# Optimization experiments

Measured on AMD Instinct MI355X. Metric: run time of the kernel, lower is better.

The kernel has to match this reference:

```python
import jax, jax.numpy as jnp
import numpy as np

N_HEAD = 16
E = 1024
B, T = 2, 2048


def setup_inputs() -> dict:
    key = jax.random.key(0)
    ks = jax.random.split(key, 5)
    s = 1.0 / np.sqrt(E)
    return {
        "x": jax.random.normal(ks[0], (B, T, E), dtype=jnp.float32),
        "w_qkv": jax.random.normal(ks[1], (E, 3 * E), dtype=jnp.float32) * s,
        "b_qkv": jnp.zeros((3 * E,), dtype=jnp.float32),
        "w_proj": jax.random.normal(ks[2], (E, E), dtype=jnp.float32) * s,
        "b_proj": jnp.zeros((E,), dtype=jnp.float32),
    }


def reference(x, w_qkv, b_qkv, w_proj, b_proj):
    Bsz, Tlen, Emb = x.shape
    hd = Emb // N_HEAD
    qkv = x @ w_qkv + b_qkv  # [B, T, 3E]
    q, k, v = jnp.split(qkv, 3, axis=-1)
    # [B, H, T, hd]
    q = q.reshape(Bsz, Tlen, N_HEAD, hd).transpose(0, 2, 1, 3)
    k = k.reshape(Bsz, Tlen, N_HEAD, hd).transpose(0, 2, 1, 3)
    v = v.reshape(Bsz, Tlen, N_HEAD, hd).transpose(0, 2, 1, 3)
    scale = 1.0 / jnp.sqrt(jnp.asarray(hd, dtype=x.dtype))
    scores = jnp.einsum("bhqd,bhkd->bhqk", q, k) * scale  # [B, H, T, T]
    causal = jnp.tril(jnp.ones((Tlen, Tlen), dtype=bool))
    scores = jnp.where(causal, scores, jnp.asarray(-jnp.inf, dtype=scores.dtype))
    attn = jax.nn.softmax(scores, axis=-1)
    y = jnp.einsum("bhqk,bhkd->bhqd", attn, v)  # [B, H, T, hd]
    y = y.transpose(0, 2, 1, 3).reshape(Bsz, Tlen, Emb)
    return y @ w_proj + b_proj
```

## Files before the change

kernel.cpp:

```cpp
#include <hip/hip_runtime.h>
#include <hip/hip_bf16.h>

typedef __hip_bfloat16 bf16;
typedef __attribute__((ext_vector_type(8))) short sh8;
typedef __attribute__((ext_vector_type(4))) float f32x4;

#define BB 2
#define TT 2048
#define EE 1024
#define NH 16
#define HD 64
#define M_ROWS (BB * TT)
#define PPAD 72

__device__ __forceinline__ float b2f(bf16 v) { return __bfloat162float(v); }
__device__ __forceinline__ bf16 f2b(float v) { return __float2bfloat16(v); }
__device__ __forceinline__ unsigned short f2bu(float v) {
    union { bf16 b; unsigned short u; } x; x.b = f2b(v); return x.u;
}

__device__ __forceinline__ void gl2lds16(const bf16* g, bf16* l) {
    __builtin_amdgcn_global_load_lds(
        (__attribute__((address_space(1))) void*)g,
        (__attribute__((address_space(3))) void*)l, 16, 0, 0);
}

__global__ __launch_bounds__(256) void prep(
    const float* __restrict__ x, bf16* __restrict__ xb,
    const float* __restrict__ Wq, bf16* __restrict__ Wqt,
    const float* __restrict__ Wp, bf16* __restrict__ Wpt) {
    const int bid = blockIdx.x;
    if (bid < 4096) {
        const int i = bid * 256 + threadIdx.x;
        const float4 v = ((const float4*)x)[i];
        ushort4 u;
        u.x = f2bu(v.x); u.y = f2bu(v.y); u.z = f2bu(v.z); u.w = f2bu(v.w);
        ((ushort4*)xb)[i] = u;
        return;
    }
    __shared__ float Ld[64][65];
    const float* src; bf16* dst; int ncols, nc0, kr0;
    if (bid < 4096 + 768) {
        const int t = bid - 4096;
        src = Wq; dst = Wqt; ncols = 3072;
        nc0 = (t % 48) * 64; kr0 = (t / 48) * 64;
    } else {
        const int t = bid - 4096 - 768;
        src = Wp; dst = Wpt; ncols = 1024;
        nc0 = (t % 16) * 64; kr0 = (t / 16) * 64;
    }
#pragma unroll
    for (int i = 0; i < 16; ++i) {
        const int e = threadIdx.x + i * 256;
        Ld[e >> 6][e & 63] = src[(size_t)(kr0 + (e >> 6)) * ncols + nc0 + (e & 63)];
    }
    __syncthreads();
#pragma unroll
    for (int i = 0; i < 16; ++i) {
        const int e = threadIdx.x + i * 256;
        const int r2 = e & 63, c2 = e >> 6;
        dst[(size_t)(nc0 + c2) * EE + kr0 + r2] = f2b(Ld[r2][c2]);
    }
}

__device__ __forceinline__ void mfma_gemm_core(
    const bf16* __restrict__ A, const bf16* __restrict__ Bt,
    int m0, int n0, f32x4 acc[4][4], bf16* Al, bf16* Bl) {
    const int tid = threadIdx.x, w = tid >> 6, lane = tid & 63;
    const int li = lane & 15, quad = lane >> 4;
    const int wm = (w & 1) * 64, wn = (w >> 1) * 64;
    const int srow = w * 32 + (lane >> 3);
    const int scol = (lane & 7) * 8;

#pragma unroll
    for (int mt = 0; mt < 4; ++mt)
#pragma unroll
        for (int nt = 0; nt < 4; ++nt) acc[mt][nt] = (f32x4){0.f, 0.f, 0.f, 0.f};

    for (int k0 = 0; k0 < EE; k0 += 64) {
        __syncthreads();
#pragma unroll
        for (int j = 0; j < 4; ++j) {
            const int row = srow + j * 8;
            const int sk = scol ^ ((row & 7) * 8);
            gl2lds16(A  + (size_t)(m0 + row) * EE + k0 + sk, Al + row * 64 + scol);
            gl2lds16(Bt + (size_t)(n0 + row) * EE + k0 + sk, Bl + row * 64 + scol);
        }
        __syncthreads();
#pragma unroll
        for (int ks = 0; ks < 2; ++ks) {
            const int kof = (ks * 32 + quad * 8) ^ ((li & 7) * 8);
            sh8 af[4], bv[4];
#pragma unroll
            for (int mt = 0; mt < 4; ++mt)
                af[mt] = *(const sh8*)(Al + (wm + mt * 16 + li) * 64 + kof);
#pragma unroll
            for (int nt = 0; nt < 4; ++nt)
                bv[nt] = *(const sh8*)(Bl + (wn + nt * 16 + li) * 64 + kof);
#pragma unroll
            for (int mt = 0; mt < 4; ++mt)
#pragma unroll
                for (int nt = 0; nt < 4; ++nt)
                    acc[mt][nt] = __builtin_amdgcn_mfma_f32_16x16x32_bf16(
                        af[mt], bv[nt], acc[mt][nt], 0, 0, 0);
        }
    }
}

__global__ __launch_bounds__(256) void gemm_qkv_mfma(
    const bf16* __restrict__ A, const bf16* __restrict__ Bt,
    const float* __restrict__ bias,
    bf16* __restrict__ Qb, bf16* __restrict__ Kb, bf16* __restrict__ Vb) {
    __shared__ bf16 Al[128 * 64];
    __shared__ bf16 Bl[128 * 64];
    f32x4 acc[4][4];
    const int m0 = blockIdx.y * 128, n0 = blockIdx.x * 128;
    mfma_gemm_core(A, Bt, m0, n0, acc, Al, Bl);

    const int tid = threadIdx.x, w = tid >> 6, lane = tid & 63;
    const int li = lane & 15, quad = lane >> 4;
    const int wm = (w & 1) * 64, wn = (w >> 1) * 64;
    const int which = n0 >> 10;

#pragma unroll
    for (int nt = 0; nt < 4; ++nt) {
        const int n = n0 + wn + nt * 16 + li;
        const int hseg = n & 1023;
        const int h = hseg >> 6, d = hseg & 63;
        const float bv = bias[n];
        if (which == 2) {
#pragma unroll
            for (int mt = 0; mt < 4; ++mt) {
                const int mb = m0 + wm + mt * 16 + quad * 4;
                const int b = mb >> 11, t = mb & (TT - 1);
                ushort4 u;
                u.x = f2bu(acc[mt][nt][0] + bv);
                u.y = f2bu(acc[mt][nt][1] + bv);
                u.z = f2bu(acc[mt][nt][2] + bv);
                u.w = f2bu(acc[mt][nt][3] + bv);
                *(ushort4*)(Vb + ((size_t)((b * NH + h) * HD + d)) * TT + t) = u;
            }
        } else {
            bf16* dst = (which == 0) ? Qb : Kb;
            const float scl = (which == 0) ? 0.125f : 1.0f;
#pragma unroll
            for (int mt = 0; mt < 4; ++mt)
#pragma unroll
                for (int r = 0; r < 4; ++r) {
                    const int m = m0 + wm + mt * 16 + quad * 4 + r;
                    const int b = m >> 11, t = m & (TT - 1);
                    dst[((size_t)(b * NH + h) * TT + t) * HD + d] =
                        f2b((acc[mt][nt][r] + bv) * scl);
                }
        }
    }
}

__global__ __launch_bounds__(256) void gemm_proj_mfma(
    const bf16* __restrict__ A, const bf16* __restrict__ Bt,
    const float* __restrict__ bias, float* __restrict__ C) {
    __shared__ bf16 Al[128 * 64];
    __shared__ bf16 Bl[128 * 64];
    f32x4 acc[4][4];
    const int m0 = blockIdx.y * 128, n0 = blockIdx.x * 128;
    mfma_gemm_core(A, Bt, m0, n0, acc, Al, Bl);

    const int tid = threadIdx.x, w = tid >> 6, lane = tid & 63;
    const int li = lane & 15, quad = lane >> 4;
    const int wm = (w & 1) * 64, wn = (w >> 1) * 64;

#pragma unroll
    for (int nt = 0; nt < 4; ++nt) {
        const int n = n0 + wn + nt * 16 + li;
        const float bv = bias[n];
#pragma unroll
        for (int mt = 0; mt < 4; ++mt)
#pragma unroll
            for (int r = 0; r < 4; ++r) {
                const int m = m0 + wm + mt * 16 + quad * 4 + r;
                C[(size_t)m * EE + n] = acc[mt][nt][r] + bv;
            }
    }
}

__global__ __launch_bounds__(256) void attn_mfma(
    const bf16* __restrict__ Q, const bf16* __restrict__ K,
    const bf16* __restrict__ Vt, bf16* __restrict__ Y) {
    __shared__ bf16 Kl[2][64 * 64];
    __shared__ bf16 Vl[2][64 * 64];
    __shared__ bf16 Pl[4][16 * PPAD];

    const int tid  = threadIdx.x;
    const int w    = tid >> 6;
    const int lane = tid & 63;
    const int li   = lane & 15;
    const int quad = lane >> 4;
    const int swz  = (li & 7) * 8;
    const int idx  = blockIdx.x;
    const int qb   = 31 - (idx >> 5);
    const int bh   = idx & 31;
    const int q0   = qb << 6;
    const int qw0  = q0 + w * 16;

    const bf16* Qb = Q  + (size_t)bh * TT * HD;
    const bf16* Kb = K  + (size_t)bh * TT * HD;
    const bf16* Vb = Vt + (size_t)bh * HD * TT;

    sh8 qf0 = *(const sh8*)(Qb + (size_t)(qw0 + li) * HD + quad * 8);
    sh8 qf1 = *(const sh8*)(Qb + (size_t)(qw0 + li) * HD + 32 + quad * 8);

    f32x4 o[4];
#pragma unroll
    for (int nt = 0; nt < 4; ++nt) o[nt] = (f32x4){0.f, 0.f, 0.f, 0.f};
    float lacc = 0.f;

    const int l8 = lane >> 3, l7 = lane & 7;
    const int gcol = ((l7 ^ l8) * 8);

    const int ntiles = qb + 1;
#pragma unroll
    for (int c = 0; c < 2; ++c) {
        const int rb = w * 16 + c * 8;
        gl2lds16(Kb + (size_t)(rb + l8) * HD + gcol, &Kl[0][rb * 64]);
        gl2lds16(Vb + (size_t)(rb + l8) * TT + gcol, &Vl[0][rb * 64]);
    }

    for (int it = 0; it < ntiles; ++it) {
        const int cur = it & 1;
        __syncthreads();
        if (it + 1 < ntiles) {
            const int j1 = (it + 1) << 6;
            const int nxt = cur ^ 1;
#pragma unroll
            for (int c = 0; c < 2; ++c) {
                const int rb = w * 16 + c * 8;
                gl2lds16(Kb + (size_t)(j1 + rb + l8) * HD + gcol, &Kl[nxt][rb * 64]);
                gl2lds16(Vb + (size_t)(rb + l8) * TT + j1 + gcol, &Vl[nxt][rb * 64]);
            }
        }
        const bf16* kb = &Kl[cur][0];
        const bf16* vb = &Vl[cur][0];

        const bool diag = (it == ntiles - 1);
#pragma unroll
        for (int nt = 0; nt < 4; ++nt) {
            f32x4 a = (f32x4){0.f, 0.f, 0.f, 0.f};
            sh8 kf0 = *(const sh8*)(kb + (nt * 16 + li) * 64 + ((quad * 8) ^ swz));
            a = __builtin_amdgcn_mfma_f32_16x16x32_bf16(kf0, qf0, a, 0, 0, 0);
            sh8 kf1 = *(const sh8*)(kb + (nt * 16 + li) * 64 + ((32 + quad * 8) ^ swz));
            a = __builtin_amdgcn_mfma_f32_16x16x32_bf16(kf1, qf1, a, 0, 0, 0);

            ushort4 u;
            float p0, p1, p2, p3;
            if (diag) {
                const int keyb = q0 + nt * 16 + quad * 4;
                const int qg = qw0 + li;
                p0 = (keyb + 0 > qg) ? 0.f : __expf(a[0]);
                p1 = (keyb + 1 > qg) ? 0.f : __expf(a[1]);
                p2 = (keyb + 2 > qg) ? 0.f : __expf(a[2]);
                p3 = (keyb + 3 > qg) ? 0.f : __expf(a[3]);
            } else {
                p0 = __expf(a[0]); p1 = __expf(a[1]);
                p2 = __expf(a[2]); p3 = __expf(a[3]);
            }
            lacc += (p0 + p1) + (p2 + p3);
            u.x = f2bu(p0); u.y = f2bu(p1); u.z = f2bu(p2); u.w = f2bu(p3);
            *(ushort4*)(&Pl[w][li * PPAD + nt * 16 + quad * 4]) = u;
        }

#pragma unroll
        for (int ks = 0; ks < 2; ++ks) {
            sh8 pf = *(const sh8*)(&Pl[w][li * PPAD + ks * 32 + quad * 8]);
#pragma unroll
            for (int nt = 0; nt < 4; ++nt) {
                sh8 vf = *(const sh8*)(vb + (nt * 16 + li) * 64 +
                                       ((ks * 32 + quad * 8) ^ swz));
                o[nt] = __builtin_amdgcn_mfma_f32_16x16x32_bf16(pf, vf, o[nt], 0, 0, 0);
            }
        }
    }

    lacc += __shfl_xor(lacc, 16, 64);
    lacc += __shfl_xor(lacc, 32, 64);
    float rinv[4];
#pragma unroll
    for (int r = 0; r < 4; ++r)
        rinv[r] = 1.0f / __shfl(lacc, quad * 4 + r, 64);

    const int b = bh >> 4, h = bh & 15;
#pragma unroll
    for (int nt = 0; nt < 4; ++nt)
#pragma unroll
        for (int r = 0; r < 4; ++r) {
            const int q = qw0 + quad * 4 + r;
            Y[((size_t)(b * TT + q)) * EE + h * HD + nt * 16 + li] =
                f2b(o[nt][r] * rinv[r]);
        }
}

extern "C" void kernel_launch(void* const* d_in, const int* in_sizes, int n_in,
                              void* d_out, int out_size, void* d_ws, size_t ws_size,
                              hipStream_t stream) {
    const float* x      = (const float*)d_in[0];
    const float* w_qkv  = (const float*)d_in[1];
    const float* b_qkv  = (const float*)d_in[2];
    const float* w_proj = (const float*)d_in[3];
    const float* b_proj = (const float*)d_in[4];
    float* out = (float*)d_out;

    const size_t SZ = (size_t)M_ROWS * EE;
    bf16* Q   = (bf16*)d_ws;
    bf16* K   = Q + SZ;
    bf16* V   = K + SZ;
    bf16* XB  = V + SZ;
    bf16* WQT = XB + SZ;
    bf16* WPT = WQT + 3 * SZ / 4;
    bf16* Y   = XB;

    prep<<<dim3(4096 + 768 + 256), dim3(256), 0, stream>>>(
        x, XB, w_qkv, WQT, w_proj, WPT);

    gemm_qkv_mfma<<<dim3(24, 32), dim3(256), 0, stream>>>(XB, WQT, b_qkv, Q, K, V);

    attn_mfma<<<dim3((TT / 64) * (BB * NH)), dim3(256), 0, stream>>>(Q, K, V, Y);

    gemm_proj_mfma<<<dim3(8, 32), dim3(256), 0, stream>>>(Y, WPT, b_proj, out);
}
```

Before: 185.0 us.

## Rewrite QKV GEMM as 256x256 tile, 8-wave, 8-phase pipelined kernel

Replaces the 128x128, 256-thread QKV GEMM with a 256x256-tile, 512-thread kernel that double-buffers LDS and splits each K-step into phases. Within each phase, global-to-LDS staging of the next tiles overlaps with MFMA work, separated by barriers, waitcnt and s_setprio. The goal is to hide load latency and get more reuse per tile. In exchange the grid shrinks to 192 blocks, which may underfill the device's CUs, and the hand-tuned waitcnt counts carry correctness risk.

```diff
diff --git a/kernel.cpp b/kernel.cpp
--- a/kernel.cpp
+++ b/kernel.cpp
@@ -107,21 +107,153 @@
     }
 }
 
-__global__ __launch_bounds__(256) void gemm_qkv_mfma(
+#define QBM 256
+#define QBN 256
+#define QBK 64
+#define QNT (EE / QBK)
+
+__global__ __launch_bounds__(512, 2) void gemm_qkv_8ph(
     const bf16* __restrict__ A, const bf16* __restrict__ Bt,
     const float* __restrict__ bias,
     bf16* __restrict__ Qb, bf16* __restrict__ Kb, bf16* __restrict__ Vb) {
-    __shared__ bf16 Al[128 * 64];
-    __shared__ bf16 Bl[128 * 64];
-    f32x4 acc[4][4];
-    const int m0 = blockIdx.y * 128, n0 = blockIdx.x * 128;
-    mfma_gemm_core(A, Bt, m0, n0, acc, Al, Bl);
-
-    const int tid = threadIdx.x, w = tid >> 6, lane = tid & 63;
-    const int li = lane & 15, quad = lane >> 4;
-    const int wm = (w & 1) * 64, wn = (w >> 1) * 64;
+    __shared__ bf16 Al[2][QBM * QBK];
+    __shared__ bf16 Bl[2][QBN * QBK];
+
+    const int tid  = threadIdx.x;
+    const int lane = tid & 63;
+    const int w    = tid >> 6;
+    const int li   = lane & 15, quad = lane >> 4;
+    const int wr   = w >> 2, wc = w & 3;
+    const int wm   = wr << 7, wn = wc << 6;
+    const int m0   = blockIdx.y << 8, n0 = blockIdx.x << 8;
+
+    const int srow = tid >> 3;
+    const int scol = (tid & 7) << 3;
+    const int sg   = scol ^ ((srow & 7) << 3);
+    const int swz  = (li & 7) << 3;
+    const int kof0 = (quad << 3) ^ swz;
+    const int kof1 = (32 + (quad << 3)) ^ swz;
+
+    f32x4 acc[8][4];
+#pragma unroll
+    for (int m = 0; m < 8; ++m)
+#pragma unroll
+        for (int n = 0; n < 4; ++n) acc[m][n] = (f32x4){0.f, 0.f, 0.f, 0.f};
+
+    sh8 ra[8][2];
+    sh8 rb[4][2];
+
+#define QSTAGE_A(t, h) do {                                                    \
+        const int _k0 = (t) * QBK; bf16* _lb = &Al[(t) & 1][0];                \
+        _Pragma("unroll")                                                      \
+        for (int _j = 0; _j < 2; ++_j) {                                       \
+            const int _r = ((h) << 7) + (_j << 6) + srow;                      \
+            gl2lds16(A + (size_t)(m0 + _r) * EE + _k0 + sg,                    \
+                     _lb + _r * QBK + scol);                                   \
+        }                                                                      \
+    } while (0)
+
+#define QSTAGE_B(t, h) do {                                                    \
+        const int _k0 = (t) * QBK; bf16* _lb = &Bl[(t) & 1][0];                \
+        _Pragma("unroll")                                                      \
+        for (int _j = 0; _j < 2; ++_j) {                                       \
+            const int _r = ((h) << 7) + (_j << 6) + srow;                      \
+            gl2lds16(Bt + (size_t)(n0 + _r) * EE + _k0 + sg,                   \
+                     _lb + _r * QBK + scol);                                   \
+        }                                                                      \
+    } while (0)
+
+#define QLOAD_A(cb, a) do {                                                    \
+        const bf16* _ab = &Al[cb][0];                                          \
+        _Pragma("unroll")                                                      \
+        for (int _m = 0; _m < 4; ++_m) {                                       \
+            const int _row = wm + (((a) << 2) + _m) * 16 + li;                 \
+            ra[((a) << 2) + _m][0] = *(const sh8*)(_ab + _row * QBK + kof0);   \
+            ra[((a) << 2) + _m][1] = *(const sh8*)(_ab + _row * QBK + kof1);   \
+        }                                                                      \
+    } while (0)
+
+#define QLOAD_B(cb, b) do {                                                    \
+        const bf16* _bb = &Bl[cb][0];                                          \
+        _Pragma("unroll")                                                      \
+        for (int _n = 0; _n < 2; ++_n) {                                       \
+            const int _row = wn + (((b) << 1) + _n) * 16 + li;                 \
+            rb[((b) << 1) + _n][0] = *(const sh8*)(_bb + _row * QBK + kof0);   \
+            rb[((b) << 1) + _n][1] = *(const sh8*)(_bb + _row * QBK + kof1);   \
+        }                                                                      \
+    } while (0)
+
+#define QMFMA(a, b) do {                                                       \
+        _Pragma("unroll")                                                      \
+        for (int _m = 0; _m < 4; ++_m)                                         \
+            _Pragma("unroll")                                                  \
+            for (int _n = 0; _n < 2; ++_n) {                                   \
+                acc[((a) << 2) + _m][((b) << 1) + _n] =                        \
+                    __builtin_amdgcn_mfma_f32_16x16x32_bf16(                   \
+                        ra[((a) << 2) + _m][0], rb[((b) << 1) + _n][0],        \
+                        acc[((a) << 2) + _m][((b) << 1) + _n], 0, 0, 0);       \
+                acc[((a) << 2) + _m][((b) << 1) + _n] =                        \
+                    __builtin_amdgcn_mfma_f32_16x16x32_bf16(                   \
+                        ra[((a) << 2) + _m][1], rb[((b) << 1) + _n][1],        \
+                        acc[((a) << 2) + _m][((b) << 1) + _n], 0, 0, 0);       \
+            }                                                                  \
+    } while (0)
+
+#define PH_MID() do { __builtin_amdgcn_s_barrier();                            \
+        asm volatile("s_waitcnt lgkmcnt(0)" ::: "memory");                     \
+        __builtin_amdgcn_s_setprio(1); } while (0)
+#define PH_END() do { __builtin_amdgcn_s_setprio(0);                           \
+        __builtin_amdgcn_s_barrier(); } while (0)
+#define PH_END_VM4() do { __builtin_amdgcn_s_setprio(0);                       \
+        asm volatile("s_waitcnt vmcnt(4)" ::: "memory");                       \
+        __builtin_amdgcn_s_barrier(); } while (0)
+
+    QSTAGE_A(0, 0); QSTAGE_A(0, 1); QSTAGE_B(0, 0); QSTAGE_B(0, 1);
+    QSTAGE_A(1, 0); QSTAGE_A(1, 1);
+    asm volatile("s_waitcnt vmcnt(4)" ::: "memory");
+    __builtin_amdgcn_s_barrier();
+
+#pragma unroll 1
+    for (int i = 0; i < QNT / 2 - 1; ++i) {
+        const int t1 = 2 * i + 1, t2 = 2 * i + 2, t3 = 2 * i + 3;
+        QLOAD_A(0, 0); QLOAD_B(0, 0); QSTAGE_B(t1, 0);
+        PH_MID(); QMFMA(0, 0); PH_END();
+        QLOAD_A(0, 1); QSTAGE_B(t1, 1);
+        PH_MID(); QMFMA(1, 0); PH_END();
+        QLOAD_B(0, 1); QSTAGE_A(t2, 0);
+        PH_MID(); QMFMA(0, 1); PH_END();
+        QSTAGE_A(t2, 1);
+        PH_MID(); QMFMA(1, 1); PH_END_VM4();
+        QLOAD_A(1, 0); QLOAD_B(1, 0); QSTAGE_B(t2, 0);
+        PH_MID(); QMFMA(0, 0); PH_END();
+        QLOAD_A(1, 1); QSTAGE_B(t2, 1);
+        PH_MID(); QMFMA(1, 0); PH_END();
+        QLOAD_B(1, 1); QSTAGE_A(t3, 0);
+        PH_MID(); QMFMA(0, 1); PH_END();
+        QSTAGE_A(t3, 1);
+        PH_MID(); QMFMA(1, 1); PH_END_VM4();
+    }
+
+    QSTAGE_B(QNT - 1, 0); QSTAGE_B(QNT - 1, 1);
+    QLOAD_A(0, 0); QLOAD_B(0, 0); QMFMA(0, 0);
+    QLOAD_A(0, 1); QMFMA(1, 0);
+    QLOAD_B(0, 1); QMFMA(0, 1); QMFMA(1, 1);
+    asm volatile("s_waitcnt vmcnt(0)" ::: "memory");
+    __builtin_amdgcn_s_barrier();
+    QLOAD_A(1, 0); QLOAD_B(1, 0); QMFMA(0, 0);
+    QLOAD_A(1, 1); QMFMA(1, 0);
+    QLOAD_B(1, 1); QMFMA(0, 1); QMFMA(1, 1);
+
+#undef QSTAGE_A
+#undef QSTAGE_B
+#undef QLOAD_A
+#undef QLOAD_B
+#undef QMFMA
+#undef PH_MID
+#undef PH_END
+#undef PH_END_VM4
+
     const int which = n0 >> 10;
-
 #pragma unroll
     for (int nt = 0; nt < 4; ++nt) {
         const int n = n0 + wn + nt * 16 + li;
@@ -130,7 +262,7 @@
         const float bv = bias[n];
         if (which == 2) {
 #pragma unroll
-            for (int mt = 0; mt < 4; ++mt) {
+            for (int mt = 0; mt < 8; ++mt) {
                 const int mb = m0 + wm + mt * 16 + quad * 4;
                 const int b = mb >> 11, t = mb & (TT - 1);
                 ushort4 u;
@@ -144,7 +276,7 @@
             bf16* dst = (which == 0) ? Qb : Kb;
             const float scl = (which == 0) ? 0.125f : 1.0f;
 #pragma unroll
-            for (int mt = 0; mt < 4; ++mt)
+            for (int mt = 0; mt < 8; ++mt)
 #pragma unroll
                 for (int r = 0; r < 4; ++r) {
                     const int m = m0 + wm + mt * 16 + quad * 4 + r;
@@ -320,7 +452,7 @@
     prep<<<dim3(4096 + 768 + 256), dim3(256), 0, stream>>>(
         x, XB, w_qkv, WQT, w_proj, WPT);
 
-    gemm_qkv_mfma<<<dim3(24, 32), dim3(256), 0, stream>>>(XB, WQT, b_qkv, Q, K, V);
+    gemm_qkv_8ph<<<dim3(12, 16), dim3(512), 0, stream>>>(XB, WQT, b_qkv, Q, K, V);
 
     attn_mfma<<<dim3((TT / 64) * (BB * NH)), dim3(256), 0, stream>>>(Q, K, V, Y);
 
```

After: 184.5 us. Within noise of the previous version (-0.2%).
